# Performance work log

Hardware: AMD Instinct MI355X
Metric: run time of the kernel (lower is better)

Reference implementation:

```python
import jax, jax.numpy as jnp
import numpy as np

ITERS = 4
LN_EPS = 1e-5


def build_grid(H, W):
    # standard uORF grid in [-1, 1], shape (H, W, 2), last dim = (x, y)
    x = jnp.linspace(-1.0 + 1.0 / W, 1.0 - 1.0 / W, W)
    y = jnp.linspace(-1.0 + 1.0 / H, 1.0 - 1.0 / H, H)
    yy, xx = jnp.meshgrid(y, x, indexing='ij')
    return jnp.stack([xx, yy], axis=-1)


def ln(x, g, b):
    m = jnp.mean(x, axis=-1, keepdims=True)
    v = jnp.var(x, axis=-1, keepdims=True)
    return (x - m) * jax.lax.rsqrt(v + LN_EPS) * g + b


def setup_inputs():
    key = jax.random.key(0)
    ks = jax.random.split(key, 16)
    B, H, W, C, K, Ds = 4, 64, 64, 256, 5, 256
    s = 0.02
    inp = {
        'feat': jax.random.normal(ks[0], (B, H, W, C), jnp.float32),
        'mask': (jax.random.uniform(ks[1], (K, 1, H, W)) > 0.5).astype(jnp.float32),
        'noise': jax.random.normal(ks[2], (B, K, Ds), jnp.float32),
        'slots_mu': jax.random.normal(ks[3], (1, 1, Ds), jnp.float32),
        'slots_logsigma': jax.random.normal(ks[4], (1, 1, Ds), jnp.float32) * s,
        'norm_g': jnp.ones((C,), jnp.float32), 'norm_b': jnp.zeros((C,), jnp.float32),
        'grid_W': jax.random.normal(ks[5], (C, 4), jnp.float32) * s,
        'grid_b': jnp.zeros((C,), jnp.float32),
        'k_W': jax.random.normal(ks[6], (C, C), jnp.float32) * s,
        'v_W': jax.random.normal(ks[7], (C, C), jnp.float32) * s,
        'mlp_g': jnp.ones((C,), jnp.float32), 'mlp_b': jnp.zeros((C,), jnp.float32),
        'mlp_W': jax.random.normal(ks[8], (Ds, C), jnp.float32) * s,
        'mlp_bias': jnp.zeros((Ds,), jnp.float32),
        'q_g': jnp.ones((Ds,), jnp.float32), 'q_b': jnp.zeros((Ds,), jnp.float32),
        'q_W': jax.random.normal(ks[9], (Ds, Ds), jnp.float32) * s,
        'gru_Wih': jax.random.normal(ks[10], (3 * Ds, Ds), jnp.float32) * s,
        'gru_Whh': jax.random.normal(ks[11], (3 * Ds, Ds), jnp.float32) * s,
        'gru_bih': jnp.zeros((3 * Ds,), jnp.float32),
        'gru_bhh': jnp.zeros((3 * Ds,), jnp.float32),
        'res_g': jnp.ones((Ds,), jnp.float32), 'res_b': jnp.zeros((Ds,), jnp.float32),
        'res_W': jax.random.normal(ks[12], (Ds, Ds), jnp.float32) * s,
        'res_bias': jnp.zeros((Ds,), jnp.float32),
    }
    return inp


def reference(feat, mask, noise, slots_mu, slots_logsigma, norm_g, norm_b,
              grid_W, grid_b, k_W, v_W, mlp_g, mlp_b, mlp_W, mlp_bias,
              q_g, q_b, q_W, gru_Wih, gru_Whh, gru_bih, gru_bhh,
              res_g, res_b, res_W, res_bias):
    B, H, W, C = feat.shape
    K = mask.shape[0]
    N = H * W
    Ds = slots_mu.shape[-1]
    scale = Ds ** -0.5

    grid = build_grid(H, W)                                   # (H, W, 2)
    # foreground positions: mask-weighted mean of grid -> (K, 2)
    g = jnp.transpose(grid, (2, 0, 1))[None]                  # (1, 2, H, W)
    fg_pos = jnp.sum(g * mask, axis=(2, 3)) / (jnp.sum(mask, axis=(2, 3)) + 1e-5)
    fg_pos = jnp.broadcast_to(fg_pos[None], (B, K, 2))        # (B, K, 2)

    feat_n = ln(feat.reshape(B, N, C), norm_g, norm_b)        # (B, N, C)
    mask_flat = mask.reshape(K, N)
    slot = slots_mu + jnp.exp(slots_logsigma) * noise         # (B, K, Ds)

    # k, v with relative position embedding; fg_pos never changes in-loop,
    # so compute once (the original recomputes the same values each iter).
    rel = grid.reshape(1, 1, N, 2) - fg_pos[:, :, None, :]    # (B, K, N, 2)
    rel4 = jnp.concatenate([rel, -rel], axis=-1)              # (B, K, N, 4)
    ge = rel4 @ grid_W.T + grid_b                             # (B, K, N, C)
    kbase = feat_n @ k_W.T                                    # (B, N, C)
    vbase = feat_n @ v_W.T
    kk = ln(kbase[:, None] + ge, mlp_g, mlp_b) @ mlp_W.T + mlp_bias  # (B,K,N,Ds)
    vv = ln(vbase[:, None] + ge, mlp_g, mlp_b) @ mlp_W.T + mlp_bias

    attn_vis = None
    for _ in range(ITERS):
        slot_prev = slot
        q = ln(slot, q_g, q_b) @ q_W.T                        # (B, K, Ds)
        attn = jnp.einsum('bkd,bknd->bkn', q, kk) * scale
        attn = jnp.where(mask_flat[None] == 0, -1e9, attn)
        attn = jax.nn.softmax(attn, axis=-1)                  # (B, K, N)
        upd = jnp.einsum('bkn,bknd->bkd', attn, vv)           # (B, K, Ds)
        # torch GRUCell
        x = upd.reshape(-1, Ds)
        h = slot.reshape(-1, Ds)
        gi = x @ gru_Wih.T + gru_bih
        gh = h @ gru_Whh.T + gru_bhh
        ir, iz, inn = jnp.split(gi, 3, axis=-1)
        hr, hz, hn = jnp.split(gh, 3, axis=-1)
        r = jax.nn.sigmoid(ir + hr)
        z = jax.nn.sigmoid(iz + hz)
        n = jnp.tanh(inn + r * hn)
        hnew = ((1.0 - z) * n + z * h).reshape(B, K, Ds)
        slot = (ln(hnew, res_g, res_b) @ res_W.T + res_bias) + slot_prev
        amin = attn.min(axis=-1, keepdims=True)
        amax = attn.max(axis=-1, keepdims=True)
        attn_vis = (attn - amin) / (amax - amin + 1e-5)
    return slot, fg_pos, attn_vis
```

## Files before the change

### kernel.cpp

```cpp
#include <hip/hip_runtime.h>
#include <math.h>

typedef unsigned short u16;
typedef unsigned int   u32;
typedef short bf8v __attribute__((ext_vector_type(8)));
typedef float f4v  __attribute__((ext_vector_type(4)));

static constexpr int B_=4, C_=256, K_=5, D_=256, N_=4096, IT_=4;
static constexpr float EPS_=1e-5f;
static constexpr int P0_MISC=96, P0_UQ=97, P0_FG=98, P0_GRID=103;
static constexpr int BT_QP=512, BT_TR=532, BT_GRID=660;

__device__ __forceinline__ float bf2f(u16 u){ u32 x=((u32)u)<<16; float f; __builtin_memcpy(&f,&x,4); return f; }
__device__ __forceinline__ float bflo(u32 u){ u32 x=u<<16; float f; __builtin_memcpy(&f,&x,4); return f; }
__device__ __forceinline__ float bfhi(u32 u){ u32 x=u&0xffff0000u; float f; __builtin_memcpy(&f,&x,4); return f; }
__device__ __forceinline__ u16 f2bf(float f){ u32 x; __builtin_memcpy(&x,&f,4); u32 r=x+0x7fffu+((x>>16)&1u); return (u16)(r>>16); }
__device__ __forceinline__ float ldin(const void* p, size_t i, int f){
  return f ? ((const float*)p)[i] : bf2f(((const u16*)p)[i]);
}
__device__ __forceinline__ void stout(void* p, size_t i, float v, int f){
  if (f) ((float*)p)[i]=v; else ((u16*)p)[i]=f2bf(v);
}
__device__ __forceinline__ int sw16(int row,int col){
  return row*256 + ((((col>>3)^(row&7))<<3) | (col&7));
}

__device__ __forceinline__ void breduce4(float&a,float&b,float&c,float&d,float* red){
  #pragma unroll
  for(int o=32;o>0;o>>=1){
    a+=__shfl_down(a,o,64); b+=__shfl_down(b,o,64);
    c+=__shfl_down(c,o,64); d+=__shfl_down(d,o,64);
  }
  int w=threadIdx.x>>6;
  __syncthreads();
  if((threadIdx.x&63)==0){ red[w]=a; red[4+w]=b; red[8+w]=c; red[12+w]=d; }
  __syncthreads();
  a=red[0]+red[1]+red[2]+red[3];
  b=red[4]+red[5]+red[6]+red[7];
  c=red[8]+red[9]+red[10]+red[11];
  d=red[12]+red[13]+red[14]+red[15];
}
__device__ __forceinline__ void breduce4_16(float&a,float&b,float&c,float&d,float* red){
  #pragma unroll
  for(int o=32;o>0;o>>=1){
    a+=__shfl_down(a,o,64); b+=__shfl_down(b,o,64);
    c+=__shfl_down(c,o,64); d+=__shfl_down(d,o,64);
  }
  int w=threadIdx.x>>6;
  __syncthreads();
  if((threadIdx.x&63)==0){ red[w]=a; red[16+w]=b; red[32+w]=c; red[48+w]=d; }
  __syncthreads();
  a=0;b=0;c=0;d=0;
  #pragma unroll
  for(int i=0;i<16;++i){ a+=red[i]; b+=red[16+i]; c+=red[32+i]; d+=red[48+i]; }
}

__device__ __forceinline__ int probe_f(const void* feat, float* red){
  const u32* p=(const u32*)feat;
  int t=threadIdx.x; int bad=0;
  #pragma unroll
  for(int s=0;s<8;++s){
    u32 wd=p[t+s*256];
    float lo=bf2f((u16)(wd&0xffffu));
    if(!(fabsf(lo)<1e6f)) bad++;
  }
  float bb=(float)bad, z1=0,z2=0,z3=0;
  breduce4(bb,z1,z2,z3,red);
  return (bb>=16.f)?1:0;
}

__global__ void prep0_kernel(const void* feat,
    const void* kW, const void* vW, const void* mW,
    const void* mu, const void* lsig, const void* noise,
    const void* gW, const void* gb_, const void* mg,
    const void* mb_, const void* mbias, const void* mask,
    int* flag, int* cnt, float* slot, float* gvec,
    u16* Wkb, u16* Wvb, u16* Wgb,
    float* Uvec, float* Qs, float* fg, void* out)
{
  __shared__ float redp[16];
  int bid=blockIdx.x;
  int t=threadIdx.x;
  int f=probe_f(feat, redp);
  if(bid==0 && t==0) *flag=f;
  __syncthreads();
  if(bid<P0_MISC){
    int which=bid>>5;
    int base=(bid&31)*2048;
    if(which==0){
      #pragma unroll
      for(int s=0;s<8;++s){ int e=base+s*256+t; Wkb[e]=f2bf(ldin(kW,e,f)); }
    } else if(which==1){
      #pragma unroll
      for(int s=0;s<8;++s){ int e=base+s*256+t; Wvb[e]=f2bf(ldin(vW,e,f)); }
    } else {
      #pragma unroll
      for(int s=0;s<8;++s){ int e=base+s*256+t; int c=e&255; Wgb[e]=f2bf(ldin(mg,c,f)*ldin(mW,e,f)); }
    }
    return;
  }
  if(bid==P0_MISC){
    if(t<16) cnt[t]=0;
    #pragma unroll
    for(int s=0;s<20;++s){ int e=s*256+t; int d=e&255;
      slot[e]=ldin(mu,d,f)+expf(ldin(lsig,d,f))*ldin(noise,e,f); }
    #pragma unroll
    for(int s=0;s<3;++s){ int e=s*256+t;
      int c=e&255, sel=e>>8;
      float v;
      if(sel==0)      v=ldin(gW,c*4+0,f)-ldin(gW,c*4+2,f);
      else if(sel==1) v=ldin(gW,c*4+1,f)-ldin(gW,c*4+3,f);
      else            v=ldin(gb_,c,f);
      gvec[e]=v;
    }
    return;
  }
  __shared__ float s_a[256], s_b[256], s_c[256];
  if(bid==P0_UQ){
    __shared__ float s_mg[256], s_mb[256];
    s_a[t]=ldin(gW,t*4+0,f)-ldin(gW,t*4+2,f);
    s_b[t]=ldin(gW,t*4+1,f)-ldin(gW,t*4+3,f);
    s_c[t]=ldin(gb_,t,f);
    s_mg[t]=ldin(mg,t,f);
    s_mb[t]=ldin(mb_,t,f);
    __syncthreads();
    float u1=0,u2=0,u3=0,gw=0,bw=0;
    if(f){
      const float4* rp=(const float4*)mW + (size_t)t*64;
      #pragma unroll 8
      for(int j=0;j<64;++j){
        float4 v4=rp[j]; int c=j*4;
        float m0=v4.x,m1=v4.y,m2=v4.z,m3=v4.w;
        float w0=s_mg[c]*m0, w1=s_mg[c+1]*m1, w2=s_mg[c+2]*m2, w3=s_mg[c+3]*m3;
        u1+=s_a[c]*w0+s_a[c+1]*w1+s_a[c+2]*w2+s_a[c+3]*w3;
        u2+=s_b[c]*w0+s_b[c+1]*w1+s_b[c+2]*w2+s_b[c+3]*w3;
        u3+=s_c[c]*w0+s_c[c+1]*w1+s_c[c+2]*w2+s_c[c+3]*w3;
        gw+=w0+w1+w2+w3;
        bw+=s_mb[c]*m0+s_mb[c+1]*m1+s_mb[c+2]*m2+s_mb[c+3]*m3;
      }
    } else {
      const bf8v* rp=(const bf8v*)((const u16*)mW + (size_t)t*256);
      #pragma unroll 8
      for(int j=0;j<32;++j){
        bf8v v8=rp[j]; int c=j*8;
        #pragma unroll
        for(int e=0;e<8;++e){
          float mwv=bf2f((u16)(unsigned short)v8[e]);
          float wg=s_mg[c+e]*mwv;
          u1+=s_a[c+e]*wg; u2+=s_b[c+e]*wg; u3+=s_c[c+e]*wg; gw+=wg;
          bw+=s_mb[c+e]*mwv;
        }
      }
    }
    Uvec[t]=u1; Uvec[256+t]=u2; Uvec[512+t]=u3; Uvec[768+t]=gw;
    Uvec[1024+t]=bw+ldin(mbias,t,f);
    float a=s_a[t], b=s_b[t], cc=s_c[t];
    float s0=a*a,s1=b*b,s2=cc*cc,s3=a*b; breduce4(s0,s1,s2,s3,redp);
    float s4=a*cc,s5=b*cc,s6=a,s7=b;     breduce4(s4,s5,s6,s7,redp);
    float s8=cc,z1=0,z2=0,z3=0;          breduce4(s8,z1,z2,z3,redp);
    if(t==0){
      Qs[0]=s0; Qs[1]=s1; Qs[2]=s2; Qs[3]=s3; Qs[4]=s4; Qs[5]=s5;
      Qs[6]=s6*(1.f/256.f); Qs[7]=s7*(1.f/256.f); Qs[8]=s8*(1.f/256.f);
    }
  } else {
    int k=bid-P0_FG;
    float sx=0,sy=0,sm=0;
    #pragma unroll
    for(int s=0;s<16;++s){
      int p=t+s*256;
      float m=ldin(mask,(size_t)k*N_+p,f);
      int i=p>>6, j=p&63;
      float x=(2*j+1)*(1.0f/64.0f)-1.0f;
      float y=(2*i+1)*(1.0f/64.0f)-1.0f;
      sx+=x*m; sy+=y*m; sm+=m;
    }
    float d=0;
    breduce4(sx,sy,sm,d,redp);
    if(t==0){
      float inv=1.0f/(sm+1e-5f);
      float fx=sx*inv, fy=sy*inv;
      fg[k*2]=fx; fg[k*2+1]=fy;
      for(int b=0;b<B_;++b){
        stout(out, 5120+(b*K_+k)*2+0, fx, f);
        stout(out, 5120+(b*K_+k)*2+1, fy, f);
      }
    }
  }
}

__global__ void __launch_bounds__(512,4) base_kernel(const int* flag, const void* feat, const void* ng, const void* nb,
    const u16* Wkb, const u16* Wvb, const u16* Wgb, const float* gvec,
    float* scal, u16* PkT, u16* Pvb,
    const float* slot, const void* qg, const void* qb_, const void* qW,
    const void* rW, const void* Wih, const void* Whh,
    u16* WqT, u16* WrT, u16* WihT, u16* WhhT,
    float* qbuf)
{
  extern __shared__ u16 smem[];
  u16* bufA = smem;
  u16* bufB = smem + 8192;
  int t=threadIdx.x, f=*flag;
  if(blockIdx.x>=BT_TR){
    float (*tile)[65] = (float(*)[65])smem;
    int b2=blockIdx.x-BT_TR;
    const void* src; u16* dst; int OS;
    if(b2<16){ src=qW; dst=WqT; OS=256; }
    else if(b2<32){ src=rW; dst=WrT; OS=256; b2-=16; }
    else if(b2<80){ src=Wih; dst=WihT; OS=768; b2-=32; }
    else { src=Whh; dst=WhhT; OS=768; b2-=80; }
    int r0=(b2>>2)*64, c0=(b2&3)*64;
    int lane=t&63, wv=t>>6;
    #pragma unroll
    for(int it=0;it<8;++it){
      int i=wv*8+it;
      tile[i][lane]=ldin(src,(size_t)(r0+i)*256+c0+lane,f);
    }
    __syncthreads();
    #pragma unroll
    for(int it=0;it<8;++it){
      int i=wv*8+it;
      dst[(size_t)(c0+i)*OS + r0 + lane] = f2bf(tile[lane][i]);
    }
    return;
  }
  if(blockIdx.x>=BT_QP){
    float* Lq =(float*)smem;
    float* pp =(float*)smem+256;
    float* red=(float*)smem+768;
    int bk=blockIdx.x-BT_QP;
    int tt=t&255, hh=t>>8, w=t>>6;
    float x=slot[bk*256+tt];
    float s=x, s2=x*x;
    #pragma unroll
    for(int o=32;o>0;o>>=1){ s+=__shfl_down(s,o,64); s2+=__shfl_down(s2,o,64); }
    if((t&63)==0){ red[w]=s; red[8+w]=s2; }
    __syncthreads();
    s=0; s2=0;
    #pragma unroll
    for(int i=0;i<8;++i){ s+=red[i]; s2+=red[8+i]; }
    float m=s*(1.f/512.f), v=s2*(1.f/512.f)-m*m;
    float lq=(x-m)*rsqrtf(v+EPS_)*ldin(qg,tt,f)+ldin(qb_,tt,f);
    if(hh==0) Lq[tt]=lq;
    __syncthreads();
    float acc=0; int cb=hh*128;
    if(f){
      const float4* rp=(const float4*)qW + ((size_t)tt*256+cb)/4;
      #pragma unroll 8
      for(int j=0;j<32;++j){
        float4 v4=rp[j]; int c=cb+j*4;
        acc+=Lq[c]*v4.x+Lq[c+1]*v4.y+Lq[c+2]*v4.z+Lq[c+3]*v4.w;
      }
    } else {
      const bf8v* rp=(const bf8v*)((const u16*)qW + (size_t)tt*256+cb);
      #pragma unroll 8
      for(int j=0;j<16;++j){
        bf8v v8=rp[j]; int c=cb+j*8;
        #pragma unroll
        for(int e=0;e<8;++e) acc+=Lq[c+e]*bf2f((u16)(unsigned short)v8[e]);
      }
    }
    pp[hh*256+tt]=acc;
    __syncthreads();
    if(hh==0) qbuf[bk*256+tt]=pp[tt]+pp[256+tt];
    return;
  }
  int w=t>>6, l=t&63;
  int quad=l>>4, m=l&15;
  int row0=blockIdx.x*32;
  {
    float g0=ldin(ng,4*l+0,f), g1=ldin(ng,4*l+1,f), g2=ldin(ng,4*l+2,f), g3=ldin(ng,4*l+3,f);
    float b0=ldin(nb,4*l+0,f), b1=ldin(nb,4*l+1,f), b2=ldin(nb,4*l+2,f), b3=ldin(nb,4*l+3,f);
    #pragma unroll
    for(int r4=0;r4<4;++r4){
      int row=4*w+r4;
      float x0,x1,x2,x3;
      if(f){
        float4 v4=((const float4*)feat)[(size_t)(row0+row)*64+l];
        x0=v4.x; x1=v4.y; x2=v4.z; x3=v4.w;
      } else {
        ushort4 uu=((const ushort4*)feat)[(size_t)(row0+row)*64+l];
        x0=bf2f(uu.x); x1=bf2f(uu.y); x2=bf2f(uu.z); x3=bf2f(uu.w);
      }
      float s=x0+x1+x2+x3, s2=x0*x0+x1*x1+x2*x2+x3*x3;
      #pragma unroll
      for(int o=32;o>0;o>>=1){ s+=__shfl_xor(s,o,64); s2+=__shfl_xor(s2,o,64); }
      float mm=s*(1.f/256.f), inv=rsqrtf(s2*(1.f/256.f)-mm*mm+EPS_);
      ushort4 o4=make_ushort4(f2bf((x0-mm)*inv*g0+b0), f2bf((x1-mm)*inv*g1+b1),
                              f2bf((x2-mm)*inv*g2+b2), f2bf((x3-mm)*inv*g3+b3));
      *(ushort4*)&bufA[sw16(row,4*l)]=o4;
    }
  }
  __syncthreads();
  {
    f4v ack[2][2], acv[2][2];
    #pragma unroll
    for(int rt=0;rt<2;++rt)
      #pragma unroll
      for(int i=0;i<2;++i){ ack[rt][i]=(f4v){0.f,0.f,0.f,0.f}; acv[rt][i]=(f4v){0.f,0.f,0.f,0.f}; }
    #pragma unroll
    for(int kk=0;kk<8;++kk){
      int kcol=kk*32+quad*8;
      bf8v af[2];
      #pragma unroll
      for(int rt=0;rt<2;++rt) af[rt]=*(bf8v*)&bufA[sw16(rt*16+m,kcol)];
      #pragma unroll
      for(int i=0;i<2;++i){
        int n=w*32+16*i+m;
        bf8v bk=*(const bf8v*)(Wkb+(size_t)n*256+kcol);
        bf8v bv=*(const bf8v*)(Wvb+(size_t)n*256+kcol);
        #pragma unroll
        for(int rt=0;rt<2;++rt){
          ack[rt][i]=__builtin_amdgcn_mfma_f32_16x16x32_bf16(af[rt],bk,ack[rt][i],0,0,0);
          acv[rt][i]=__builtin_amdgcn_mfma_f32_16x16x32_bf16(af[rt],bv,acv[rt][i],0,0,0);
        }
      }
    }
    #pragma unroll
    for(int rt=0;rt<2;++rt)
      #pragma unroll
      for(int i=0;i<2;++i){
        int n=w*32+16*i+m;
        #pragma unroll
        for(int r=0;r<4;++r)
          bufB[sw16(rt*16+quad*4+r,n)]=f2bf(ack[rt][i][r]);
      }
    __syncthreads();
    #pragma unroll
    for(int rt=0;rt<2;++rt)
      #pragma unroll
      for(int i=0;i<2;++i){
        int n=w*32+16*i+m;
        #pragma unroll
        for(int r=0;r<4;++r)
          bufA[sw16(rt*16+quad*4+r,n)]=f2bf(acv[rt][i][r]);
      }
  }
  __syncthreads();
  {
    float gA0=gvec[l], gA1=gvec[l+64], gA2=gvec[l+128], gA3=gvec[l+192];
    float gB0=gvec[256+l], gB1=gvec[256+l+64], gB2=gvec[256+l+128], gB3=gvec[256+l+192];
    float gC0=gvec[512+l], gC1=gvec[512+l+64], gC2=gvec[512+l+128], gC3=gvec[512+l+192];
    for(int r4=0;r4<4;++r4){
      int row=4*w+r4;
      float k0=bf2f(bufB[sw16(row,l)]),     k1=bf2f(bufB[sw16(row,l+64)]),
            k2=bf2f(bufB[sw16(row,l+128)]), k3=bf2f(bufB[sw16(row,l+192)]);
      float x0=bf2f(bufA[sw16(row,l)]),     x1=bf2f(bufA[sw16(row,l+64)]),
            x2=bf2f(bufA[sw16(row,l+128)]), x3=bf2f(bufA[sw16(row,l+192)]);
      float v0=k0+k1+k2+k3;
      float v1=k0*k0+k1*k1+k2*k2+k3*k3;
      float v2=k0*gA0+k1*gA1+k2*gA2+k3*gA3;
      float v3=k0*gB0+k1*gB1+k2*gB2+k3*gB3;
      float v4=k0*gC0+k1*gC1+k2*gC2+k3*gC3;
      float v5=x0+x1+x2+x3;
      float v6=x0*x0+x1*x1+x2*x2+x3*x3;
      float v7=x0*gA0+x1*gA1+x2*gA2+x3*gA3;
      float v8=x0*gB0+x1*gB1+x2*gB2+x3*gB3;
      float v9=x0*gC0+x1*gC1+x2*gC2+x3*gC3;
      #pragma unroll
      for(int o=32;o>0;o>>=1){
        v0+=__shfl_down(v0,o,64); v1+=__shfl_down(v1,o,64); v2+=__shfl_down(v2,o,64);
        v3+=__shfl_down(v3,o,64); v4+=__shfl_down(v4,o,64); v5+=__shfl_down(v5,o,64);
        v6+=__shfl_down(v6,o,64); v7+=__shfl_down(v7,o,64); v8+=__shfl_down(v8,o,64);
        v9+=__shfl_down(v9,o,64);
      }
      if(l==0){
        float* sc=scal+(size_t)(row0+row)*10;
        sc[0]=v0; sc[1]=v1; sc[2]=v2; sc[3]=v3; sc[4]=v4;
        sc[5]=v5; sc[6]=v6; sc[7]=v7; sc[8]=v8; sc[9]=v9;
      }
    }
  }
  {
    f4v apk[2][2], apv[2][2];
    #pragma unroll
    for(int rt=0;rt<2;++rt)
      #pragma unroll
      for(int i=0;i<2;++i){ apk[rt][i]=(f4v){0.f,0.f,0.f,0.f}; apv[rt][i]=(f4v){0.f,0.f,0.f,0.f}; }
    #pragma unroll
    for(int kk=0;kk<8;++kk){
      int kcol=kk*32+quad*8;
      bf8v afk[2], afv[2];
      #pragma unroll
      for(int rt=0;rt<2;++rt){
        afk[rt]=*(bf8v*)&bufB[sw16(rt*16+m,kcol)];
        afv[rt]=*(bf8v*)&bufA[sw16(rt*16+m,kcol)];
      }
      #pragma unroll
      for(int i=0;i<2;++i){
        int n=w*32+16*i+m;
        bf8v bg=*(const bf8v*)(Wgb+(size_t)n*256+kcol);
        #pragma unroll
        for(int rt=0;rt<2;++rt){
          apk[rt][i]=__builtin_amdgcn_mfma_f32_16x16x32_bf16(afk[rt],bg,apk[rt][i],0,0,0);
          apv[rt][i]=__builtin_amdgcn_mfma_f32_16x16x32_bf16(afv[rt],bg,apv[rt][i],0,0,0);
        }
      }
    }
    __syncthreads();
    #pragma unroll
    for(int rt=0;rt<2;++rt)
      #pragma unroll
      for(int i=0;i<2;++i){
        int d=w*32+16*i+m;
        #pragma unroll
        for(int r=0;r<4;++r){
          bufA[sw16(rt*16+quad*4+r,d)]=f2bf(apk[rt][i][r]);
          bufB[sw16(rt*16+quad*4+r,d)]=f2bf(apv[rt][i][r]);
        }
      }
  }
  __syncthreads();
  #pragma unroll
  for(int r4=0;r4<4;++r4){
    int row=4*w+r4;
    ushort4 k4=*(ushort4*)&bufA[sw16(row,4*l)];
    ushort4 s4=*(ushort4*)&bufB[sw16(row,4*l)];
    *(ushort4*)(PkT+(size_t)(row0+row)*256+4*l)=k4;
    *(ushort4*)(Pvb+(size_t)(row0+row)*256+4*l)=s4;
  }
}

__global__ void __launch_bounds__(512) attn_kernel(const int* flag, const float* qbuf, const u16* PkT,
    const float* scal, const float* Qs, const float* Uvec, const float* fg, const void* mask,
    const u16* Pvb, float* logits, float* pmax, float* psum, float* updpart, float* sscp,
    int store_lg)
{
  __shared__ float q5[1280];
  __shared__ float un[10240];
  __shared__ float lgs[320], ivs[320], mvs[320];
  __shared__ float qs5[40], fgs[10], Qss[9], MSl[5];
  __shared__ float sred[8][5][4];
  int tid=threadIdx.x, f=*flag;
  int b=blockIdx.x>>6, ch=blockIdx.x&63;
  int w=tid>>6, l=tid&63;
  int n0=ch<<6;
  for(int p=tid;p<1280;p+=512) q5[p]=qbuf[(size_t)b*1280+p];
  if(tid<10) fgs[tid]=fg[tid];
  if(tid<9)  Qss[tid]=Qs[tid];
  __syncthreads();
  for(int p=w;p<25;p+=8){
    int k=p/5, j=p%5;
    float s=q5[k*256+l]*Uvec[j*256+l]+q5[k*256+l+64]*Uvec[j*256+l+64]
           +q5[k*256+l+128]*Uvec[j*256+l+128]+q5[k*256+l+192]*Uvec[j*256+l+192];
    #pragma unroll
    for(int o=32;o>0;o>>=1) s+=__shfl_xor(s,o,64);
    if(l==0) qs5[k*8+j]=s;
  }
  {
    int n=n0+l; size_t row=(size_t)b*N_+n;
    float dk0=0,dk1=0,dk2=0,dk3=0,dk4=0;
    int cbase=w*32;
    const u16* kp=PkT+row*256+cbase;
    #pragma unroll
    for(int v=0;v<4;++v){
      bf8v k8=*(const bf8v*)(kp+v*8);
      #pragma unroll
      for(int e=0;e<8;++e){
        int c=cbase+v*8+e;
        float pv=bf2f((u16)(unsigned short)k8[e]);
        dk0+=pv*q5[c]; dk1+=pv*q5[256+c]; dk2+=pv*q5[512+c];
        dk3+=pv*q5[768+c]; dk4+=pv*q5[1024+c];
      }
    }
    un[(w*5+0)*64+l]=dk0; un[(w*5+1)*64+l]=dk1; un[(w*5+2)*64+l]=dk2;
    un[(w*5+3)*64+l]=dk3; un[(w*5+4)*64+l]=dk4;
  }
  __syncthreads();
  if(tid<320){
    int k=tid>>6, nl=tid&63;
    float dot=0;
    #pragma unroll
    for(int j=0;j<8;++j) dot+=un[(j*5+k)*64+nl];
    int n2=n0+nl; size_t row2=(size_t)b*N_+n2;
    const float* sc=scal+row2*10;
    float rx=(2*(n2&63)+1)*(1.f/64.f)-1.f-fgs[2*k];
    float ry=(2*(n2>>6)+1)*(1.f/64.f)-1.f-fgs[2*k+1];
    float qge=rx*rx*Qss[0]+ry*ry*Qss[1]+Qss[2]+2.f*(rx*ry*Qss[3]+rx*Qss[4]+ry*Qss[5]);
    float mk=sc[0]*(1.f/256.f)+rx*Qss[6]+ry*Qss[7]+Qss[8];
    float sxk=sc[1]+2.f*(rx*sc[2]+ry*sc[3]+sc[4])+qge;
    float invK=rsqrtf(sxk*(1.f/256.f)-mk*mk+EPS_);
    float lg=invK*(dot+rx*qs5[k*8+0]+ry*qs5[k*8+1]+qs5[k*8+2]-mk*qs5[k*8+3])+qs5[k*8+4];
    float mval=ldin(mask,(size_t)k*N_+n2,f);
    lg=(mval==0.f)? -1e9f : lg*0.0625f;
    if(store_lg) logits[((size_t)(b*5+k))*N_+n2]=lg;
    lgs[tid]=lg;
    float mv=sc[5]*(1.f/256.f)+rx*Qss[6]+ry*Qss[7]+Qss[8];
    float sxv=sc[6]+2.f*(rx*sc[7]+ry*sc[8]+sc[9])+qge;
    mvs[tid]=mv;
    ivs[tid]=rsqrtf(sxv*(1.f/256.f)-mv*mv+EPS_);
  }
  __syncthreads();
  if(tid<64){
    #pragma unroll
    for(int k=0;k<5;++k){
      float v=lgs[k*64+tid];
      float M=v;
      #pragma unroll
      for(int o=32;o>0;o>>=1) M=fmaxf(M,__shfl_xor(M,o,64));
      float e=expf(v-M);
      #pragma unroll
      for(int o=32;o>0;o>>=1) e+=__shfl_xor(e,o,64);
      if(tid==0){ pmax[((size_t)(b*64+ch))*5+k]=M; psum[((size_t)(b*64+ch))*5+k]=e; MSl[k]=M; }
    }
  }
  __syncthreads();
  {
    float acc[5][4]={{0}};
    float swx[5]={0,0,0,0,0}, swy[5]={0,0,0,0,0}, sw[5]={0,0,0,0,0}, swm[5]={0,0,0,0,0};
    #pragma unroll 2
    for(int rr=0;rr<8;++rr){
      int nl=w*8+rr; int n2=n0+nl;
      size_t row=(size_t)b*N_+n2;
      uint2 pu=*(const uint2*)(Pvb+row*256+l*4);
      float px=bflo(pu.x), py=bfhi(pu.x), pz=bflo(pu.y), pw=bfhi(pu.y);
      int jx=n2&63, iy=n2>>6;
      #pragma unroll
      for(int k=0;k<5;++k){
        float wgt=expf(lgs[k*64+nl]-MSl[k])*ivs[k*64+nl];
        float rx=(2*jx+1)*(1.f/64.f)-1.f-fgs[2*k];
        float ry=(2*iy+1)*(1.f/64.f)-1.f-fgs[2*k+1];
        acc[k][0]+=wgt*px; acc[k][1]+=wgt*py; acc[k][2]+=wgt*pz; acc[k][3]+=wgt*pw;
        sw[k]+=wgt; swx[k]+=wgt*rx; swy[k]+=wgt*ry; swm[k]+=wgt*mvs[k*64+nl];
      }
    }
    #pragma unroll
    for(int k=0;k<5;++k)
      *(float4*)&un[(w*5+k)*256+l*4]=make_float4(acc[k][0],acc[k][1],acc[k][2],acc[k][3]);
    if(l==0){
      #pragma unroll
      for(int k=0;k<5;++k){ sred[w][k][0]=swx[k]; sred[w][k][1]=swy[k];
                            sred[w][k][2]=sw[k];  sred[w][k][3]=swm[k]; }
    }
  }
  __syncthreads();
  for(int p=tid;p<1280;p+=512){
    int k=p>>8, d=p&255;
    float v=0;
    #pragma unroll
    for(int j=0;j<8;++j) v+=un[(j*5+k)*256+d];
    updpart[((size_t)blockIdx.x*5+k)*256+d]=v;
  }
  if(tid<20){
    int kk=tid>>2, j=tid&3;
    float s=0;
    #pragma unroll
    for(int jj=0;jj<8;++jj) s+=sred[jj][kk][j];
    sscp[((size_t)blockIdx.x*5+kk)*4+j]=s;
  }
}

__global__ void __launch_bounds__(1024) gru_kernel(const int* flag, float* slot, const float* updpart,
    const float* sscp, const float* Uvec, const float* pmax, const float* psum, const float* logits,
    const u16* WihT, const u16* WhhT, const void* bih, const void* bhh,
    const void* rg, const void* rb_, const u16* WrT, const void* rbias,
    const void* qg, const void* qb_, const u16* WqT, float* qbuf,
    int do_vis, void* out)
{
  __shared__ float u[256], h[256], sn[256];
  __shared__ float part[4][6][256];
  __shared__ float red[64];
  __shared__ float cvec[4];
  __shared__ float fch[64];
  __shared__ float MSg[2];
  int tid=threadIdx.x, t=tid&255, g=tid>>8;
  int blk=blockIdx.x;
  int f=*flag;
  if(blk>=20){
    if(!do_vis) return;
    int bk2=blk-20, k2=bk2%K_, b2=bk2/K_;
    if(tid<64){
      float pm=pmax[((size_t)(b2*64+tid))*5+k2];
      float ps=psum[((size_t)(b2*64+tid))*5+k2];
      float M=pm;
      #pragma unroll
      for(int o=32;o>0;o>>=1) M=fmaxf(M,__shfl_xor(M,o,64));
      float e=ps*expf(pm-M);
      #pragma unroll
      for(int o=32;o>0;o>>=1) e+=__shfl_xor(e,o,64);
      if(tid==0){ MSg[0]=M; MSg[1]=1.0f/e; }
    }
    __syncthreads();
    float M=MSg[0], Sinv=MSg[1];
    float a[4]; float mn=1e30f, mx=-1e30f;
    #pragma unroll
    for(int s=0;s<4;++s){
      a[s]=expf(logits[(size_t)bk2*N_+tid+s*1024]-M)*Sinv;
      mn=fminf(mn,a[s]); mx=fmaxf(mx,a[s]);
    }
    #pragma unroll
    for(int o=32;o>0;o>>=1){ mn=fminf(mn,__shfl_down(mn,o,64)); mx=fmaxf(mx,__shfl_down(mx,o,64)); }
    int wv=tid>>6;
    __syncthreads();
    if((tid&63)==0){ red[wv]=mn; red[16+wv]=mx; }
    __syncthreads();
    mn=1e30f; mx=-1e30f;
    #pragma unroll
    for(int i=0;i<16;++i){ mn=fminf(mn,red[i]); mx=fmaxf(mx,red[16+i]); }
    float inv=1.0f/(mx-mn+1e-5f);
    #pragma unroll
    for(int s=0;s<4;++s) stout(out, 5160+(size_t)bk2*N_+tid+s*1024, (a[s]-mn)*inv, f);
    return;
  }
  int bk=blk, k=bk%K_, b=bk/K_;
  if(tid<64){
    float pm=pmax[((size_t)(b*64+tid))*5+k];
    float ps=psum[((size_t)(b*64+tid))*5+k];
    float M=pm;
    #pragma unroll
    for(int o=32;o>0;o>>=1) M=fmaxf(M,__shfl_xor(M,o,64));
    float fc=expf(pm-M);
    fch[tid]=fc;
    float e=ps*fc;
    #pragma unroll
    for(int o=32;o>0;o>>=1) e+=__shfl_xor(e,o,64);
    if(tid==0){ MSg[0]=M; MSg[1]=1.0f/e; }
  }
  __syncthreads();
  float Sinv=MSg[1];
  float ua=0;
  {
    int ch0=g*16;
    #pragma unroll 4
    for(int ci=0;ci<16;++ci){ int ch=ch0+ci; ua += fch[ch]*updpart[(((size_t)(b*64+ch))*5+k)*256+t]; }
  }
  part[g][0][t]=ua;
  if(t<4){
    float s=0;
    #pragma unroll 4
    for(int ci=0;ci<16;++ci){ int ch=g*16+ci; s += fch[ch]*sscp[(((size_t)(b*64+ch))*5+k)*4+t]; }
    part[g][1][t]=s;
  }
  __syncthreads();
  if(g==0 && t<4) cvec[t]=part[0][1][t]+part[1][1][t]+part[2][1][t]+part[3][1][t];
  __syncthreads();
  if(g==0){
    float uu=part[0][0][t]+part[1][0][t]+part[2][0][t]+part[3][0][t];
    u[t]=(uu+cvec[0]*Uvec[t]+cvec[1]*Uvec[256+t]+cvec[2]*Uvec[512+t]-cvec[3]*Uvec[768+t])*Sinv
         +Uvec[1024+t];
    h[t]=slot[bk*256+t];
  }
  __syncthreads();
  float p0=0,p1=0,p2=0,p3=0,p4=0,p5=0;
  int c0=g*64;
  #pragma unroll 8
  for(int cc=0;cc<64;++cc){
    int c=c0+cc;
    float uc=u[c], hc=h[c];
    const u16* wi=WihT+(size_t)c*768+t;
    const u16* wh=WhhT+(size_t)c*768+t;
    p0+=uc*bf2f(wi[0]); p1+=uc*bf2f(wi[256]); p2+=uc*bf2f(wi[512]);
    p3+=hc*bf2f(wh[0]); p4+=hc*bf2f(wh[256]); p5+=hc*bf2f(wh[512]);
  }
  part[g][0][t]=p0; part[g][1][t]=p1; part[g][2][t]=p2;
  part[g][3][t]=p3; part[g][4][t]=p4; part[g][5][t]=p5;
  __syncthreads();
  float hn=0;
  if(g==0){
    float gi0=ldin(bih,t,f)+part[0][0][t]+part[1][0][t]+part[2][0][t]+part[3][0][t];
    float gi1=ldin(bih,256+t,f)+part[0][1][t]+part[1][1][t]+part[2][1][t]+part[3][1][t];
    float gi2=ldin(bih,512+t,f)+part[0][2][t]+part[1][2][t]+part[2][2][t]+part[3][2][t];
    float gh0=ldin(bhh,t,f)+part[0][3][t]+part[1][3][t]+part[2][3][t]+part[3][3][t];
    float gh1=ldin(bhh,256+t,f)+part[0][4][t]+part[1][4][t]+part[2][4][t]+part[3][4][t];
    float gh2=ldin(bhh,512+t,f)+part[0][5][t]+part[1][5][t]+part[2][5][t]+part[3][5][t];
    float r=1.f/(1.f+expf(-(gi0+gh0)));
    float z=1.f/(1.f+expf(-(gi1+gh1)));
    float nn=tanhf(gi2+r*gh2);
    hn=(1.f-z)*nn+z*h[t];
  }
  float s=hn, sq=hn*hn, za=0, zb=0;
  breduce4_16(s,sq,za,zb,red);
  if(g==0){
    float m=s*(1.f/256.f), var=sq*(1.f/256.f)-m*m;
    u[t]=(hn-m)*rsqrtf(var+EPS_)*ldin(rg,t,f)+ldin(rb_,t,f);
  }
  __syncthreads();
  float pr=0;
  #pragma unroll 8
  for(int cc=0;cc<64;++cc){ int c=c0+cc; pr+=u[c]*bf2f(WrT[(size_t)c*256+t]); }
  part[g][0][t]=pr;
  __syncthreads();
  if(g==0){
    float acc=ldin(rbias,t,f)+h[t]+part[0][0][t]+part[1][0][t]+part[2][0][t]+part[3][0][t];
    slot[bk*256+t]=acc;
    stout(out, (size_t)bk*256+t, acc, f);
    sn[t]=acc;
  }
  __syncthreads();
  float xs=(g==0)? sn[t]:0.f;
  float xq=xs*xs, zc=0, zd=0;
  breduce4_16(xs,xq,zc,zd,red);
  if(g==0){
    float m=xs*(1.f/256.f), var=xq*(1.f/256.f)-m*m;
    u[t]=(sn[t]-m)*rsqrtf(var+EPS_)*ldin(qg,t,f)+ldin(qb_,t,f);
  }
  __syncthreads();
  float pq=0;
  #pragma unroll 8
  for(int cc=0;cc<64;++cc){ int c=c0+cc; pq+=u[c]*bf2f(WqT[(size_t)c*256+t]); }
  part[g][0][t]=pq;
  __syncthreads();
  if(g==0){
    float qv=part[0][0][t]+part[1][0][t]+part[2][0][t]+part[3][0][t];
    qbuf[bk*256+t]=qv;
  }
}

extern "C" void kernel_launch(void* const* d_in, const int* in_sizes, int n_in,
                              void* d_out, int out_size, void* d_ws, size_t ws_size,
                              hipStream_t stream)
{
  const void* feat =d_in[0];  const void* mask =d_in[1];  const void* noise=d_in[2];
  const void* mu   =d_in[3];  const void* lsig =d_in[4];  const void* ng   =d_in[5];
  const void* nb   =d_in[6];  const void* gW   =d_in[7];  const void* gb_  =d_in[8];
  const void* kW   =d_in[9];  const void* vW   =d_in[10]; const void* mg   =d_in[11];
  const void* mb_  =d_in[12]; const void* mW   =d_in[13]; const void* mbias=d_in[14];
  const void* qg   =d_in[15]; const void* qb_  =d_in[16]; const void* qW   =d_in[17];
  const void* Wih  =d_in[18]; const void* Whh  =d_in[19]; const void* bih  =d_in[20];
  const void* bhh  =d_in[21]; const void* rg   =d_in[22]; const void* rb_  =d_in[23];
  const void* rW   =d_in[24]; const void* rbias=d_in[25];

  char* p=(char*)d_ws;
  auto alloc=[&](size_t bytes)->char*{ char* r=p; p+=(bytes+255)&~(size_t)255; return r; };
  int*   flag   =(int*)  alloc(256);
  int*   cnt    =(int*)  alloc(2048);
  float* fg     =(float*)alloc(64);
  float* slot   =(float*)alloc(5120*4);
  float* qbuf   =(float*)alloc(5120*4);
  float* logits =(float*)alloc((size_t)81920*4);
  float* pmax   =(float*)alloc(1280*4);
  float* psum   =(float*)alloc(1280*4);
  float* updpart=(float*)alloc((size_t)256*5*256*4);
  float* sscp   =(float*)alloc((size_t)256*5*4*4);
  u16*   WqT    =(u16*)  alloc((size_t)65536*2);
  u16*   WrT    =(u16*)  alloc((size_t)65536*2);
  u16*   WihT   =(u16*)  alloc((size_t)196608*2);
  u16*   WhhT   =(u16*)  alloc((size_t)196608*2);
  float* gvec   =(float*)alloc(768*4);
  float* Uvec   =(float*)alloc(1280*4);
  float* Qs     =(float*)alloc(64);
  float* scal   =(float*)alloc((size_t)163840*4);
  u16*   Wkb    =(u16*)  alloc((size_t)65536*2);
  u16*   Wvb    =(u16*)  alloc((size_t)65536*2);
  u16*   Wgb    =(u16*)  alloc((size_t)65536*2);
  u16*   PkT    =(u16*)  alloc((size_t)16384*256*2);
  u16*   Pvb    =(u16*)  alloc((size_t)16384*256*2);

  prep0_kernel<<<P0_GRID,256,0,stream>>>(feat,kW,vW,mW,mu,lsig,noise,gW,gb_,mg,
                                         mb_,mbias,mask,
                                         flag,cnt,slot,gvec,Wkb,Wvb,Wgb,
                                         Uvec,Qs,fg,d_out);
  base_kernel<<<BT_GRID,512,32768,stream>>>(flag,feat,ng,nb,Wkb,Wvb,Wgb,gvec,scal,PkT,Pvb,
                                            slot,qg,qb_,qW,rW,Wih,Whh,
                                            WqT,WrT,WihT,WhhT,qbuf);
  for(int it=0; it<IT_; ++it){
    attn_kernel<<<B_*64,512,0,stream>>>(flag,qbuf,PkT,scal,Qs,Uvec,fg,mask,Pvb,
                                        logits,pmax,psum,updpart,sscp,(it==IT_-1)?1:0);
    int nb_g = (it==IT_-1)? 40 : 20;
    gru_kernel<<<nb_g,1024,0,stream>>>(flag,slot,updpart,sscp,Uvec,pmax,psum,logits,
                                       WihT,WhhT,bih,bhh,rg,rb_,WrT,rbias,
                                       qg,qb_,WqT,qbuf,(it==IT_-1)?1:0,d_out);
  }
}
```

Before: 323.2 us.

## Fold GRU slot update into the next attention kernel launch

Every attention block now redundantly recomputes the previous iteration's softmax combine, GRU cell, residual MLP and query projection for its batch, instead of running a separate small gru_kernel between attention launches. Partial buffers and slot buffers are ping-ponged so a launch can read the previous iteration's partials while writing its own. This removes three serial launches of a low-occupancy kernel and their global round trips. In exchange, each of the 256 blocks repeats the same matrix-vector work and weight reads, which adds per-block latency before the attention phase starts.

```diff
diff --git a/kernel.cpp b/kernel.cpp
--- a/kernel.cpp
+++ b/kernel.cpp
@@ -74,7 +74,7 @@
     const void* mu, const void* lsig, const void* noise,
     const void* gW, const void* gb_, const void* mg,
     const void* mb_, const void* mbias, const void* mask,
-    int* flag, int* cnt, float* slot, float* gvec,
+    int* flag, float* slot, float* gvec,
     u16* Wkb, u16* Wvb, u16* Wgb,
     float* Uvec, float* Qs, float* fg, void* out)
 {
@@ -100,7 +100,6 @@
     return;
   }
   if(bid==P0_MISC){
-    if(t<16) cnt[t]=0;
     #pragma unroll
     for(int s=0;s<20;++s){ int e=s*256+t; int d=e&255;
       slot[e]=ldin(mu,d,f)+expf(ldin(lsig,d,f))*ldin(noise,e,f); }
@@ -423,7 +422,12 @@
 __global__ void __launch_bounds__(512) attn_kernel(const int* flag, const float* qbuf, const u16* PkT,
     const float* scal, const float* Qs, const float* Uvec, const float* fg, const void* mask,
     const u16* Pvb, float* logits, float* pmax, float* psum, float* updpart, float* sscp,
-    int store_lg)
+    int store_lg, int fold,
+    const float* pmaxP, const float* psumP, const float* updpartP, const float* sscpP,
+    const float* slotP, float* slotN,
+    const u16* WihT, const u16* WhhT, const void* bih, const void* bhh,
+    const void* rg, const void* rb_, const u16* WrT, const void* rbias,
+    const void* qg, const void* qb_, const u16* WqT)
 {
   __shared__ float q5[1280];
   __shared__ float un[10240];
@@ -434,9 +438,186 @@
   int b=blockIdx.x>>6, ch=blockIdx.x&63;
   int w=tid>>6, l=tid&63;
   int n0=ch<<6;
-  for(int p=tid;p<1280;p+=512) q5[p]=qbuf[(size_t)b*1280+p];
   if(tid<10) fgs[tid]=fg[tid];
   if(tid<9)  Qss[tid]=Qs[tid];
+  if(fold){
+    float* uL  = un;
+    float* hL  = un+1280;
+    float* pgL = un+2560;
+    float* cvf = (float*)sred;
+    if(tid<320){
+      int k=tid>>6, c2=tid&63;
+      float pm=pmaxP[((size_t)(b*64+c2))*5+k];
+      float ps=psumP[((size_t)(b*64+c2))*5+k];
+      float M=pm;
+      #pragma unroll
+      for(int o=32;o>0;o>>=1) M=fmaxf(M,__shfl_xor(M,o,64));
+      float fc=expf(pm-M);
+      lgs[tid]=fc;
+      float e=ps*fc;
+      #pragma unroll
+      for(int o=32;o>0;o>>=1) e+=__shfl_xor(e,o,64);
+      if(c2==0){ qs5[k]=M; qs5[5+k]=1.0f/e; }
+    }
+    __syncthreads();
+    for(int p=tid;p<1280;p+=512){
+      int k=p>>8, d=p&255;
+      float acc=0;
+      #pragma unroll 4
+      for(int c2=0;c2<64;++c2)
+        acc += lgs[k*64+c2]*updpartP[(((size_t)(b*64+c2))*5+k)*256+d];
+      uL[p]=acc;
+    }
+    if(tid<20){
+      int kk=tid>>2, j=tid&3;
+      float s=0;
+      #pragma unroll 4
+      for(int c2=0;c2<64;++c2)
+        s += lgs[kk*64+c2]*sscpP[(((size_t)(b*64+c2))*5+kk)*4+j];
+      cvf[tid]=s;
+    }
+    __syncthreads();
+    for(int p=tid;p<1280;p+=512){
+      int k=p>>8, d=p&255;
+      const float* cv=cvf+k*4;
+      uL[p]=(uL[p]+cv[0]*Uvec[d]+cv[1]*Uvec[256+d]+cv[2]*Uvec[512+d]-cv[3]*Uvec[768+d])*qs5[5+k]
+            +Uvec[1024+d];
+      hL[p]=slotP[(size_t)b*1280+p];
+    }
+    __syncthreads();
+    {
+      int g=tid>>8, t2=tid&255, c0=g*128;
+      float a0[5],a1[5],a2[5],a3[5];
+      #pragma unroll
+      for(int k=0;k<5;++k){ a0[k]=0; a1[k]=0; a2[k]=0; a3[k]=0; }
+      #pragma unroll 4
+      for(int cc=0;cc<128;++cc){
+        int c=c0+cc;
+        const u16* wi=WihT+(size_t)c*768+t2;
+        const u16* wh=WhhT+(size_t)c*768+t2;
+        float w0=bf2f(wi[0]), w1=bf2f(wi[256]), w2=bf2f(wi[512]);
+        float v0=bf2f(wh[0]), v1=bf2f(wh[256]), v2=bf2f(wh[512]);
+        #pragma unroll
+        for(int k=0;k<5;++k){
+          float uk=uL[k*256+c], hk=hL[k*256+c];
+          a0[k]+=uk*w0+hk*v0;
+          a1[k]+=uk*w1+hk*v1;
+          a2[k]+=uk*w2;
+          a3[k]+=hk*v2;
+        }
+      }
+      if(g==0){
+        #pragma unroll
+        for(int k=0;k<5;++k){
+          pgL[(k*4+0)*256+t2]=a0[k]; pgL[(k*4+1)*256+t2]=a1[k];
+          pgL[(k*4+2)*256+t2]=a2[k]; pgL[(k*4+3)*256+t2]=a3[k];
+        }
+      }
+      __syncthreads();
+      if(g==1){
+        #pragma unroll
+        for(int k=0;k<5;++k){
+          pgL[(k*4+0)*256+t2]+=a0[k]; pgL[(k*4+1)*256+t2]+=a1[k];
+          pgL[(k*4+2)*256+t2]+=a2[k]; pgL[(k*4+3)*256+t2]+=a3[k];
+        }
+      }
+      __syncthreads();
+    }
+    for(int p=tid;p<1280;p+=512){
+      int k=p>>8, t2=p&255;
+      float g0=pgL[(k*4+0)*256+t2]+ldin(bih,t2,f)+ldin(bhh,t2,f);
+      float g1=pgL[(k*4+1)*256+t2]+ldin(bih,256+t2,f)+ldin(bhh,256+t2,f);
+      float g2=pgL[(k*4+2)*256+t2]+ldin(bih,512+t2,f);
+      float g3=pgL[(k*4+3)*256+t2]+ldin(bhh,512+t2,f);
+      float r=1.f/(1.f+expf(-g0));
+      float z=1.f/(1.f+expf(-g1));
+      float nn=tanhf(g2+r*g3);
+      uL[p]=(1.f-z)*nn+z*hL[p];
+    }
+    __syncthreads();
+    if(tid<320){
+      int k=tid>>6, lane=tid&63;
+      float s=0,s2=0;
+      #pragma unroll
+      for(int e=0;e<4;++e){ float v=uL[k*256+lane*4+e]; s+=v; s2+=v*v; }
+      #pragma unroll
+      for(int o=32;o>0;o>>=1){ s+=__shfl_xor(s,o,64); s2+=__shfl_xor(s2,o,64); }
+      if(lane==0){ float m=s*(1.f/256.f); qs5[10+k]=m; qs5[15+k]=rsqrtf(s2*(1.f/256.f)-m*m+EPS_); }
+    }
+    __syncthreads();
+    for(int p=tid;p<1280;p+=512){
+      int k=p>>8, t2=p&255;
+      hL[p]=(uL[p]-qs5[10+k])*qs5[15+k]*ldin(rg,t2,f)+ldin(rb_,t2,f);
+    }
+    __syncthreads();
+    {
+      int g=tid>>8, t2=tid&255, c0=g*128;
+      float a[5]={0,0,0,0,0};
+      #pragma unroll 4
+      for(int cc=0;cc<128;++cc){
+        int c=c0+cc;
+        float wr=bf2f(WrT[(size_t)c*256+t2]);
+        #pragma unroll
+        for(int k=0;k<5;++k) a[k]+=hL[k*256+c]*wr;
+      }
+      if(g==0){
+        #pragma unroll
+        for(int k=0;k<5;++k) pgL[k*256+t2]=a[k];
+      }
+      __syncthreads();
+      if(g==1){
+        #pragma unroll
+        for(int k=0;k<5;++k) pgL[k*256+t2]+=a[k];
+      }
+      __syncthreads();
+    }
+    for(int p=tid;p<1280;p+=512){
+      int t2=p&255;
+      float sn2=ldin(rbias,t2,f)+slotP[(size_t)b*1280+p]+pgL[p];
+      uL[p]=sn2;
+      if(ch==0) slotN[(size_t)b*1280+p]=sn2;
+    }
+    __syncthreads();
+    if(tid<320){
+      int k=tid>>6, lane=tid&63;
+      float s=0,s2=0;
+      #pragma unroll
+      for(int e=0;e<4;++e){ float v=uL[k*256+lane*4+e]; s+=v; s2+=v*v; }
+      #pragma unroll
+      for(int o=32;o>0;o>>=1){ s+=__shfl_xor(s,o,64); s2+=__shfl_xor(s2,o,64); }
+      if(lane==0){ float m=s*(1.f/256.f); qs5[10+k]=m; qs5[15+k]=rsqrtf(s2*(1.f/256.f)-m*m+EPS_); }
+    }
+    __syncthreads();
+    for(int p=tid;p<1280;p+=512){
+      int k=p>>8, t2=p&255;
+      hL[p]=(uL[p]-qs5[10+k])*qs5[15+k]*ldin(qg,t2,f)+ldin(qb_,t2,f);
+    }
+    __syncthreads();
+    {
+      int g=tid>>8, t2=tid&255, c0=g*128;
+      float a[5]={0,0,0,0,0};
+      #pragma unroll 4
+      for(int cc=0;cc<128;++cc){
+        int c=c0+cc;
+        float wq=bf2f(WqT[(size_t)c*256+t2]);
+        #pragma unroll
+        for(int k=0;k<5;++k) a[k]+=hL[k*256+c]*wq;
+      }
+      if(g==0){
+        #pragma unroll
+        for(int k=0;k<5;++k) pgL[k*256+t2]=a[k];
+      }
+      __syncthreads();
+      if(g==1){
+        #pragma unroll
+        for(int k=0;k<5;++k) pgL[k*256+t2]+=a[k];
+      }
+      __syncthreads();
+    }
+    for(int p=tid;p<1280;p+=512) q5[p]=pgL[p];
+  } else {
+    for(int p=tid;p<1280;p+=512) q5[p]=qbuf[(size_t)b*1280+p];
+  }
   __syncthreads();
   for(int p=w;p<25;p+=8){
     int k=p/5, j=p%5;
@@ -722,15 +903,19 @@
   char* p=(char*)d_ws;
   auto alloc=[&](size_t bytes)->char*{ char* r=p; p+=(bytes+255)&~(size_t)255; return r; };
   int*   flag   =(int*)  alloc(256);
-  int*   cnt    =(int*)  alloc(2048);
   float* fg     =(float*)alloc(64);
-  float* slot   =(float*)alloc(5120*4);
+  float* slotA  =(float*)alloc(5120*4);
+  float* slotB  =(float*)alloc(5120*4);
   float* qbuf   =(float*)alloc(5120*4);
   float* logits =(float*)alloc((size_t)81920*4);
-  float* pmax   =(float*)alloc(1280*4);
-  float* psum   =(float*)alloc(1280*4);
-  float* updpart=(float*)alloc((size_t)256*5*256*4);
-  float* sscp   =(float*)alloc((size_t)256*5*4*4);
+  float* pmaxA  =(float*)alloc(1280*4);
+  float* pmaxB  =(float*)alloc(1280*4);
+  float* psumA  =(float*)alloc(1280*4);
+  float* psumB  =(float*)alloc(1280*4);
+  float* updA   =(float*)alloc((size_t)256*5*256*4);
+  float* updB   =(float*)alloc((size_t)256*5*256*4);
+  float* sscpA  =(float*)alloc((size_t)256*5*4*4);
+  float* sscpB  =(float*)alloc((size_t)256*5*4*4);
   u16*   WqT    =(u16*)  alloc((size_t)65536*2);
   u16*   WrT    =(u16*)  alloc((size_t)65536*2);
   u16*   WihT   =(u16*)  alloc((size_t)196608*2);
@@ -747,17 +932,28 @@
 
   prep0_kernel<<<P0_GRID,256,0,stream>>>(feat,kW,vW,mW,mu,lsig,noise,gW,gb_,mg,
                                          mb_,mbias,mask,
-                                         flag,cnt,slot,gvec,Wkb,Wvb,Wgb,
+                                         flag,slotA,gvec,Wkb,Wvb,Wgb,
                                          Uvec,Qs,fg,d_out);
   base_kernel<<<BT_GRID,512,32768,stream>>>(flag,feat,ng,nb,Wkb,Wvb,Wgb,gvec,scal,PkT,Pvb,
-                                            slot,qg,qb_,qW,rW,Wih,Whh,
+                                            slotA,qg,qb_,qW,rW,Wih,Whh,
                                             WqT,WrT,WihT,WhhT,qbuf);
-  for(int it=0; it<IT_; ++it){
-    attn_kernel<<<B_*64,512,0,stream>>>(flag,qbuf,PkT,scal,Qs,Uvec,fg,mask,Pvb,
-                                        logits,pmax,psum,updpart,sscp,(it==IT_-1)?1:0);
-    int nb_g = (it==IT_-1)? 40 : 20;
-    gru_kernel<<<nb_g,1024,0,stream>>>(flag,slot,updpart,sscp,Uvec,pmax,psum,logits,
-                                       WihT,WhhT,bih,bhh,rg,rb_,WrT,rbias,
-                                       qg,qb_,WqT,qbuf,(it==IT_-1)?1:0,d_out);
-  }
-}
+  attn_kernel<<<B_*64,512,0,stream>>>(flag,qbuf,PkT,scal,Qs,Uvec,fg,mask,Pvb,
+                                      logits,pmaxA,psumA,updA,sscpA,0,0,
+                                      pmaxA,psumA,updA,sscpA,slotA,slotB,
+                                      WihT,WhhT,bih,bhh,rg,rb_,WrT,rbias,qg,qb_,WqT);
+  attn_kernel<<<B_*64,512,0,stream>>>(flag,qbuf,PkT,scal,Qs,Uvec,fg,mask,Pvb,
+                                      logits,pmaxB,psumB,updB,sscpB,0,1,
+                                      pmaxA,psumA,updA,sscpA,slotA,slotB,
+                                      WihT,WhhT,bih,bhh,rg,rb_,WrT,rbias,qg,qb_,WqT);
+  attn_kernel<<<B_*64,512,0,stream>>>(flag,qbuf,PkT,scal,Qs,Uvec,fg,mask,Pvb,
+                                      logits,pmaxA,psumA,updA,sscpA,0,1,
+                                      pmaxB,psumB,updB,sscpB,slotB,slotA,
+                                      WihT,WhhT,bih,bhh,rg,rb_,WrT,rbias,qg,qb_,WqT);
+  attn_kernel<<<B_*64,512,0,stream>>>(flag,qbuf,PkT,scal,Qs,Uvec,fg,mask,Pvb,
+                                      logits,pmaxB,psumB,updB,sscpB,1,1,
+                                      pmaxA,psumA,updA,sscpA,slotA,slotB,
+                                      WihT,WhhT,bih,bhh,rg,rb_,WrT,rbias,qg,qb_,WqT);
+  gru_kernel<<<40,1024,0,stream>>>(flag,slotB,updB,sscpB,Uvec,pmaxB,psumB,logits,
+                                   WihT,WhhT,bih,bhh,rg,rb_,WrT,rbias,
+                                   qg,qb_,WqT,qbuf,1,d_out);
+}
```

Measured after the change: 588.8 us. +82.2%, slower.
